# Kernel optimization log

Measured on AMD Instinct MI355X. Metric: run time of the kernel, lower is better.

Reference implementation:

```python
import jax, jax.numpy as jnp
import numpy as np
from jax import lax

B = 256
C1 = 256          # conv1 channels
NUM_CAPS = 32     # primary capsule types
CAP_DIM = 8       # primary capsule dim
NUM_PRIMARY = NUM_CAPS * 6 * 6  # 1152
NUM_OUT = 10
OUT_DIM = 16
NUM_ROUTING = 3


def squash(v):
    # v: (..., d)
    sq = jnp.sum(v * v, axis=-1, keepdims=True)
    scale = sq / (1.0 + sq)
    return scale * v / jnp.sqrt(sq + 1e-8)


def setup_inputs() -> dict:
    key = jax.random.key(0)
    k = jax.random.split(key, 6)
    x = jax.random.normal(k[0], (B, 1, 28, 28), dtype=jnp.float32)
    # kaiming fan_out init for convs
    conv1_w = jax.random.normal(k[1], (C1, 1, 9, 9), dtype=jnp.float32) * np.sqrt(2.0 / (C1 * 81))
    conv1_b = jnp.zeros((C1,), dtype=jnp.float32)
    pc_out = NUM_CAPS * CAP_DIM  # 256
    pc_w = jax.random.normal(k[2], (pc_out, C1, 9, 9), dtype=jnp.float32) * np.sqrt(2.0 / (pc_out * 81))
    pc_b = jnp.zeros((pc_out,), dtype=jnp.float32)
    W_digit = jax.random.normal(k[3], (NUM_PRIMARY, CAP_DIM, NUM_OUT, OUT_DIM), dtype=jnp.float32) * 0.01
    return {"x": x, "conv1_w": conv1_w, "conv1_b": conv1_b,
            "pc_w": pc_w, "pc_b": pc_b, "W_digit": W_digit}


def _conv(x, w, b, stride):
    y = lax.conv_general_dilated(x, w, (stride, stride), 'VALID',
                                 dimension_numbers=('NCHW', 'OIHW', 'NCHW'))
    return y + b[None, :, None, None]


def reference(x, conv1_w, conv1_b, pc_w, pc_b, W_digit):
    # conv1 + ReLU: (B,1,28,28) -> (B,256,20,20)
    h = jax.nn.relu(_conv(x, conv1_w, conv1_b, 1))
    # primary caps conv: -> (B, 256, 6, 6)
    p = _conv(h, pc_w, pc_b, 2)
    bsz, _, oh, ow = p.shape
    # (B, num_caps, cap_dim, H, W) -> (B, num_caps, H, W, cap_dim) -> (B, N, d)
    p = p.reshape(bsz, NUM_CAPS, CAP_DIM, oh, ow)
    p = jnp.transpose(p, (0, 1, 3, 4, 2)).reshape(bsz, NUM_CAPS * oh * ow, CAP_DIM)
    u = squash(p)  # (B, 1152, 8)
    # dynamic routing
    u_hat = jnp.einsum('bid,idjo->bijo', u, W_digit)  # (B, 1152, 10, 16)
    b_logits = jnp.zeros((bsz, NUM_PRIMARY, NUM_OUT, 1), dtype=u_hat.dtype)
    v = None
    for it in range(NUM_ROUTING):
        c = jax.nn.softmax(b_logits, axis=2)
        s = jnp.sum(c * u_hat, axis=1)          # (B, 10, 16)
        v = squash(s)
        if it < NUM_ROUTING - 1:
            agreement = jnp.sum(u_hat * v[:, None, :, :], axis=-1, keepdims=True)
            b_logits = b_logits + agreement
    return v
```

## Files before the change

### kernel.cpp

```cpp
#include <hip/hip_runtime.h>
#include <hip/hip_bf16.h>

#define NI 1152

typedef __attribute__((ext_vector_type(8))) _Float16 f16x8;
typedef __attribute__((ext_vector_type(4))) float f32x4;
typedef __attribute__((ext_vector_type(8))) unsigned short u16x8;
typedef __attribute__((ext_vector_type(4))) unsigned short u16x4;

static const size_t UHAT_OFF = 0;
static const size_t W6_OFF   = 0;
static const size_t H3_OFF   = 10747904UL;
static const size_t WT1_OFF  = 63176704UL;
static const size_t PP_OFF   = 63259648UL;
static const size_t U_OFF    = 94371840UL;
static const size_t SP_OFF   = 103809024UL;
static const size_t L_OFF    = 127401984UL;
static const size_t V_OFF    = 139198464UL;

__device__ __forceinline__ unsigned short f2bf(float x) {
    unsigned u = __builtin_bit_cast(unsigned, x);
    u += 0x7fffu + ((u >> 16) & 1u);
    return (unsigned short)(u >> 16);
}
__device__ __forceinline__ float bf2f(unsigned short h) {
    return __builtin_bit_cast(float, (unsigned)h << 16);
}
__device__ __forceinline__ void atomAddF(float* p, float v) {
    __hip_atomic_fetch_add(p, v, __ATOMIC_RELAXED, __HIP_MEMORY_SCOPE_AGENT);
}

__global__ __launch_bounds__(256) void k_prep_w(const float* __restrict__ pcw,
                                                _Float16* __restrict__ w6) {
    __shared__ float sl[5184];
    int oc  = blockIdx.x;
    int ic0 = blockIdx.y * 64;
    const float* src = pcw + (size_t)oc * 20736 + (size_t)ic0 * 81;
    for (int j = threadIdx.x; j < 5184; j += 256) sl[j] = src[j];
    __syncthreads();
    int og = oc >> 4, fr = oc & 15;
    for (int t = threadIdx.x; t < 5184; t += 256) {
        int tap = t >> 6, i = t & 63;
        int ic = ic0 + i;
        int ks = ic >> 5, kch = (ic >> 3) & 3, icl = ic & 7;
        int lane = kch * 16 + fr;
        w6[(((size_t)(tap * 8 + ks) * 16 + og) * 64 + lane) * 8 + icl] =
            (_Float16)sl[i * 81 + tap];
    }
}

__global__ void k_transpose_w1(const float* __restrict__ w, float* __restrict__ wT) {
    int t = blockIdx.x, oc = threadIdx.x;
    wT[t * 256 + oc] = w[oc * 81 + t];
}

__global__ __launch_bounds__(256) void k_conv1(const float* __restrict__ x,
                                               const float* __restrict__ wT1,
                                               const float* __restrict__ bias,
                                               _Float16* __restrict__ h3) {
    __shared__ _Float16 hs[2][20][256];
    int b  = blockIdx.y;
    int rp = blockIdx.x;
    int oc = threadIdx.x;
    int oy0 = rp * 2;
    const float* xb = x + (size_t)b * 784;
    float bv = bias[oc];
    float acc0[20], acc1[20];
#pragma unroll
    for (int i = 0; i < 20; ++i) { acc0[i] = bv; acc1[i] = bv; }
    for (int ky = 0; ky < 9; ++ky) {
        const float* r0 = xb + (oy0 + ky) * 28;
        const float* r1 = r0 + 28;
        float x0[28], x1[28];
#pragma unroll
        for (int c = 0; c < 28; ++c) { x0[c] = r0[c]; x1[c] = r1[c]; }
#pragma unroll
        for (int kx = 0; kx < 9; ++kx) {
            float w = wT1[(ky * 9 + kx) * 256 + oc];
#pragma unroll
            for (int px = 0; px < 20; ++px) {
                acc0[px] += x0[px + kx] * w;
                acc1[px] += x1[px + kx] * w;
            }
        }
    }
#pragma unroll
    for (int px = 0; px < 20; ++px) {
        hs[0][px][oc] = (_Float16)fmaxf(acc0[px], 0.f);
        hs[1][px][oc] = (_Float16)fmaxf(acc1[px], 0.f);
    }
    __syncthreads();
    for (int cid = threadIdx.x; cid < 1280; cid += 256) {
        int kp = cid & 31;
        int pos = cid >> 5;
        int ry = pos / 20, px2 = pos % 20;
        int ks = kp >> 2, p = kp & 3;
        f16x8 val = *(const f16x8*)&hs[ry][px2][ks * 32 + p * 8];
        _Float16* dst = h3 + ((size_t)((ks * 400 + (oy0 + ry) * 20 + px2) * 4 + p) * 256 + b) * 8;
        *(f16x8*)dst = val;
    }
}

__global__ __launch_bounds__(256, 2) void k_conv2_direct(
    const _Float16* __restrict__ h3, const _Float16* __restrict__ w6,
    float* __restrict__ pp) {
    const int blk = blockIdx.x;
    const int ks = blk & 7;
    const int rest = blk >> 3;
    const int mt = rest % 72;
    const int nt = rest / 72;
    const int pos = mt >> 1, bhalf = mt & 1;
    const int py = pos / 6, px = pos % 6;
    const int l = threadIdx.x & 63;
    const int w = threadIdx.x >> 6;
    const int wm = w >> 1, wn = w & 1;
    const int p = l >> 4, fr = l & 15;

    const _Float16* abase = h3 + (size_t)ks * 3276800 + p * 2048 +
                            (bhalf * 128 + wm * 64 + fr) * 8;
    const _Float16* bbase = w6 + (nt * 8 + wn * 4) * 512 + l * 8;

    f16x8 a[3][4], b[3][4];
    f32x4 acc[4][4];
    const f32x4 z = {0.f, 0.f, 0.f, 0.f};
#pragma unroll
    for (int mi = 0; mi < 4; ++mi)
#pragma unroll
        for (int ni = 0; ni < 4; ++ni) acc[mi][ni] = z;

#define LOADAB(buf, tap)                                                       \
    do {                                                                       \
        const int _t = (tap);                                                  \
        const int _y = _t / 9, _x = _t - _y * 9;                               \
        const _Float16* _ab = abase + ((2 * py + _y) * 20 + (2 * px + _x)) * 8192; \
        a[buf][0] = *(const f16x8*)(_ab);                                      \
        a[buf][1] = *(const f16x8*)(_ab + 128);                                \
        a[buf][2] = *(const f16x8*)(_ab + 256);                                \
        a[buf][3] = *(const f16x8*)(_ab + 384);                                \
        const _Float16* _bb = bbase + (size_t)(_t * 8 + ks) * 8192;            \
        b[buf][0] = *(const f16x8*)(_bb);                                      \
        b[buf][1] = *(const f16x8*)(_bb + 512);                                \
        b[buf][2] = *(const f16x8*)(_bb + 1024);                               \
        b[buf][3] = *(const f16x8*)(_bb + 1536);                               \
    } while (0)

#define MFMA_ALL(buf)                                                          \
    do {                                                                       \
        _Pragma("unroll") for (int mi = 0; mi < 4; ++mi)                       \
            _Pragma("unroll") for (int ni = 0; ni < 4; ++ni)                   \
                acc[mi][ni] = __builtin_amdgcn_mfma_f32_16x16x32_f16(          \
                    a[buf][mi], b[buf][ni], acc[buf == buf ? mi : mi][ni], 0, 0, 0); \
    } while (0)

#undef MFMA_ALL
#define MFMA_ALL(buf)                                                          \
    do {                                                                       \
        _Pragma("unroll") for (int mi = 0; mi < 4; ++mi)                       \
            _Pragma("unroll") for (int ni = 0; ni < 4; ++ni)                   \
                acc[mi][ni] = __builtin_amdgcn_mfma_f32_16x16x32_f16(          \
                    a[buf][mi], b[buf][ni], acc[mi][ni], 0, 0, 0);             \
    } while (0)

    LOADAB(0, 0);
    LOADAB(1, 1);
    for (int k = 0; k < 27; ++k) {
        const int t0 = 3 * k;
        LOADAB(2, t0 + 2);
        MFMA_ALL(0);
        if (t0 + 3 < 81) LOADAB(0, t0 + 3);
        MFMA_ALL(1);
        if (t0 + 4 < 81) LOADAB(1, t0 + 4);
        MFMA_ALL(2);
    }
#undef LOADAB
#undef MFMA_ALL

    const int row0 = (l >> 4) * 4;
    const int ncol = l & 15;
#pragma unroll
    for (int mi = 0; mi < 4; ++mi)
#pragma unroll
        for (int ni = 0; ni < 4; ++ni) {
            int n = nt * 128 + wn * 64 + ni * 16 + ncol;
#pragma unroll
            for (int reg = 0; reg < 4; ++reg) {
                int m = pos * 256 + bhalf * 128 + wm * 64 + mi * 16 + row0 + reg;
                atomAddF(&pp[(size_t)m * 256 + n], acc[mi][ni][reg]);
            }
        }
}

__global__ __launch_bounds__(256) void k_sum_squash2(const float* __restrict__ pp,
                                                     const float* __restrict__ bias,
                                                     float* __restrict__ u) {
    int m = blockIdx.x * 8 + (threadIdx.x >> 5);
    int cap = threadIdx.x & 31;
    const float* p0 = pp + (size_t)m * 256 + cap * 8;
    float s[8], sq = 0.f;
#pragma unroll
    for (int d = 0; d < 8; ++d) {
        float a = p0[d] + bias[cap * 8 + d];
        sq += a * a; s[d] = a;
    }
    float scale = sq / ((1.0f + sq) * sqrtf(sq + 1e-8f));
    int pos = m >> 8, b = m & 255;
    int i = cap * 36 + pos;
    float* up = u + ((size_t)i * 256 + b) * 8;
    ((float4*)up)[0] = make_float4(scale * s[0], scale * s[1], scale * s[2], scale * s[3]);
    ((float4*)up)[1] = make_float4(scale * s[4], scale * s[5], scale * s[6], scale * s[7]);
}

__global__ __launch_bounds__(256) void k_build_uhat(const float* __restrict__ u,
                                                    const float* __restrict__ W,
                                                    unsigned short* __restrict__ UH) {
    __shared__ float Ws[1280];
    int i = blockIdx.x;
    for (int t = threadIdx.x; t < 1280; t += 256) Ws[t] = W[(size_t)i * 1280 + t];
    __syncthreads();
    int b = threadIdx.x;
    const float* uptr = u + ((size_t)i * 256 + b) * 8;
    float u8[8];
    ((float4*)u8)[0] = ((const float4*)uptr)[0];
    ((float4*)u8)[1] = ((const float4*)uptr)[1];
#pragma unroll
    for (int j = 0; j < 10; ++j) {
        float o16[16];
#pragma unroll
        for (int o = 0; o < 16; ++o) o16[o] = 0.f;
#pragma unroll
        for (int d = 0; d < 8; ++d) {
            const float* wp = Ws + d * 160 + j * 16;
#pragma unroll
            for (int o = 0; o < 16; ++o) o16[o] += u8[d] * wp[o];
        }
        u16x8 h0, h1;
#pragma unroll
        for (int o = 0; o < 8; ++o) { h0[o] = f2bf(o16[o]); h1[o] = f2bf(o16[8 + o]); }
        unsigned short* dst = UH + ((size_t)(i * 10 + j) * 256 + b) * 16;
        *(u16x8*)dst = h0;
        *(u16x8*)(dst + 8) = h1;
    }
}

__global__ __launch_bounds__(256) void k_route_s0(const unsigned short* __restrict__ UH,
                                                  float* __restrict__ SP) {
    int it = blockIdx.x, bt = blockIdx.y;
    int b0 = bt * 64, i0 = it * 8;
    int b_l = threadIdx.x & 63;
    int og = __builtin_amdgcn_readfirstlane((int)(threadIdx.x >> 6));
    float acc[10][4];
#pragma unroll
    for (int j = 0; j < 10; ++j)
#pragma unroll
        for (int o = 0; o < 4; ++o) acc[j][o] = 0.f;
    for (int li = 0; li < 8; ++li) {
        const unsigned short* up = UH + ((size_t)(i0 + li) * 10 * 256 + b0 + b_l) * 16 + og * 4;
#pragma unroll
        for (int j = 0; j < 10; ++j) {
            u16x4 t = *(const u16x4*)(up + j * 4096);
#pragma unroll
            for (int o = 0; o < 4; ++o) acc[j][o] += bf2f(t[o]);
        }
    }
    float* sp = SP + ((size_t)it * 256 + b0 + b_l) * 160 + og * 4;
#pragma unroll
    for (int j = 0; j < 10; ++j)
        *(float4*)(sp + j * 16) = make_float4(0.1f * acc[j][0], 0.1f * acc[j][1],
                                              0.1f * acc[j][2], 0.1f * acc[j][3]);
}

__global__ __launch_bounds__(256) void k_route_as(float* __restrict__ L,
                                                  const unsigned short* __restrict__ UH,
                                                  const float* __restrict__ V,
                                                  float* __restrict__ SP,
                                                  int add, int storeL) {
    __shared__ float VL[64][165];
    __shared__ float LG[64][81];
    int it = blockIdx.x, bt = blockIdx.y;
    int b0 = bt * 64, i0 = it * 8;
    int b_l = threadIdx.x & 63;
    int ig = __builtin_amdgcn_readfirstlane((int)(threadIdx.x >> 6));
    int b_r = threadIdx.x >> 2, part = threadIdx.x & 3;
    {
        const float4* vsrc = (const float4*)(V + (size_t)(b0 + b_r) * 160 + part * 40);
#pragma unroll
        for (int q = 0; q < 10; ++q) {
            float4 vv = vsrc[q]; int c = part * 40 + q * 4;
            VL[b_r][c] = vv.x; VL[b_r][c + 1] = vv.y; VL[b_r][c + 2] = vv.z; VL[b_r][c + 3] = vv.w;
        }
        if (add) {
            const float4* lsrc = (const float4*)(L + (size_t)(b0 + b_r) * 11520 + i0 * 10 + part * 20);
#pragma unroll
            for (int q = 0; q < 5; ++q) {
                float4 t = lsrc[q]; int c = part * 20 + q * 4;
                LG[b_r][c] = t.x; LG[b_r][c + 1] = t.y; LG[b_r][c + 2] = t.z; LG[b_r][c + 3] = t.w;
            }
        }
    }
    __syncthreads();
#pragma unroll
    for (int ii = 0; ii < 2; ++ii) {
        int il = ig * 2 + ii;
        int i = i0 + il;
        const unsigned short* up = UH + ((size_t)i * 10 * 256 + b0 + b_l) * 16;
#pragma unroll
        for (int j = 0; j < 10; ++j) {
            u16x8 ua = *(const u16x8*)(up + j * 4096);
            u16x8 ub = *(const u16x8*)(up + j * 4096 + 8);
            float a = 0.f;
#pragma unroll
            for (int o = 0; o < 8; ++o) a += bf2f(ua[o]) * VL[b_l][j * 16 + o];
#pragma unroll
            for (int o = 0; o < 8; ++o) a += bf2f(ub[o]) * VL[b_l][j * 16 + 8 + o];
            float base = add ? LG[b_l][il * 10 + j] : 0.f;
            LG[b_l][il * 10 + j] = base + a;
        }
    }
    __syncthreads();
    if (storeL) {
        float4* ldst = (float4*)(L + (size_t)(b0 + b_r) * 11520 + i0 * 10 + part * 20);
#pragma unroll
        for (int q = 0; q < 5; ++q) {
            int c = part * 20 + q * 4;
            ldst[q] = make_float4(LG[b_r][c], LG[b_r][c + 1], LG[b_r][c + 2], LG[b_r][c + 3]);
        }
    }
    float acc[10][4];
#pragma unroll
    for (int j = 0; j < 10; ++j)
#pragma unroll
        for (int o = 0; o < 4; ++o) acc[j][o] = 0.f;
    for (int li = 0; li < 8; ++li) {
        float lg[10];
#pragma unroll
        for (int j = 0; j < 10; ++j) lg[j] = LG[b_l][li * 10 + j];
        float m = lg[0];
#pragma unroll
        for (int j = 1; j < 10; ++j) m = fmaxf(m, lg[j]);
        float e[10], ssum = 0.f;
#pragma unroll
        for (int j = 0; j < 10; ++j) { e[j] = __expf(lg[j] - m); ssum += e[j]; }
        float inv = 1.0f / ssum;
        const unsigned short* up = UH + ((size_t)(i0 + li) * 10 * 256 + b0 + b_l) * 16 + ig * 4;
#pragma unroll
        for (int j = 0; j < 10; ++j) {
            float cj = e[j] * inv;
            u16x4 t = *(const u16x4*)(up + j * 4096);
#pragma unroll
            for (int o = 0; o < 4; ++o) acc[j][o] += cj * bf2f(t[o]);
        }
    }
    float* sp = SP + ((size_t)it * 256 + b0 + b_l) * 160 + ig * 4;
#pragma unroll
    for (int j = 0; j < 10; ++j)
        *(float4*)(sp + j * 16) = make_float4(acc[j][0], acc[j][1], acc[j][2], acc[j][3]);
}

__global__ __launch_bounds__(256) void k_route_v(const float* __restrict__ SP,
                                                 float* __restrict__ vout) {
    int n = blockIdx.x * 256 + threadIdx.x;
    float ssum = 0.f;
    for (int t = 0; t < 144; ++t) ssum += SP[(size_t)t * 40960 + n];
    float sq = ssum * ssum;
    float tot = sq;
#pragma unroll
    for (int mask = 1; mask < 16; mask <<= 1) tot += __shfl_xor(tot, mask, 64);
    float scale = tot / ((1.0f + tot) * sqrtf(tot + 1e-8f));
    vout[n] = scale * ssum;
}

extern "C" void kernel_launch(void* const* d_in, const int* in_sizes, int n_in,
                              void* d_out, int out_size, void* d_ws, size_t ws_size,
                              hipStream_t stream) {
    (void)in_sizes; (void)n_in; (void)out_size; (void)ws_size;
    const float* x   = (const float*)d_in[0];
    const float* c1w = (const float*)d_in[1];
    const float* c1b = (const float*)d_in[2];
    const float* pcw = (const float*)d_in[3];
    const float* pcb = (const float*)d_in[4];
    const float* Wd  = (const float*)d_in[5];
    float* out = (float*)d_out;
    char* wsb  = (char*)d_ws;

    unsigned short* uh = (unsigned short*)(wsb + UHAT_OFF);
    _Float16* w6 = (_Float16*)(wsb + W6_OFF);
    _Float16* h3 = (_Float16*)(wsb + H3_OFF);
    float* wT1 = (float*)(wsb + WT1_OFF);
    float* pp  = (float*)(wsb + PP_OFF);
    float* u   = (float*)(wsb + U_OFF);
    float* sp  = (float*)(wsb + SP_OFF);
    float* lg  = (float*)(wsb + L_OFF);
    float* v   = (float*)(wsb + V_OFF);

    hipMemsetAsync(pp, 0, (size_t)9216 * 256 * sizeof(float), stream);

    k_prep_w<<<dim3(256, 4), 256, 0, stream>>>(pcw, w6);
    k_transpose_w1<<<81, 256, 0, stream>>>(c1w, wT1);
    k_conv1<<<dim3(10, 256), 256, 0, stream>>>(x, wT1, c1b, h3);
    k_conv2_direct<<<dim3(1152), 256, 0, stream>>>(h3, w6, pp);
    k_sum_squash2<<<1152, 256, 0, stream>>>(pp, pcb, u);
    k_build_uhat<<<1152, 256, 0, stream>>>(u, Wd, uh);

    k_route_s0<<<dim3(144, 4), 256, 0, stream>>>(uh, sp);
    k_route_v<<<160, 256, 0, stream>>>(sp, v);
    k_route_as<<<dim3(144, 4), 256, 0, stream>>>(lg, uh, v, sp, 0, 1);
    k_route_v<<<160, 256, 0, stream>>>(sp, v);
    k_route_as<<<dim3(144, 4), 256, 0, stream>>>(lg, uh, v, sp, 1, 0);
    k_route_v<<<160, 256, 0, stream>>>(sp, out);
}
```

Measured before the change: 438.2 us.

## Stage conv2 operand tiles through LDS with async global_load_lds double buffering

Replaces the per-wave direct global-to-register loads in the conv2 implicit GEMM with block-cooperative global_load_lds copies into double-buffered shared memory, so each A and B tile is fetched once per block and shared between waves. A barrier per tap synchronises the buffers. The occupancy hint is raised from 2 to 3 blocks per CU to offset the smaller register footprint. This adds LDS traffic and a per-tap sync, and its correctness depends on the exact lane-to-LDS layout of global_load_lds.

```diff
diff --git a/kernel.cpp b/kernel.cpp
--- a/kernel.cpp
+++ b/kernel.cpp
@@ -101,9 +101,12 @@
     }
 }
 
-__global__ __launch_bounds__(256, 2) void k_conv2_direct(
+__global__ __launch_bounds__(256, 3) void k_conv2_direct(
     const _Float16* __restrict__ h3, const _Float16* __restrict__ w6,
     float* __restrict__ pp) {
+    __shared__ _Float16 Asl[2 * 4096];
+    __shared__ _Float16 Bsl[2 * 4096];
+
     const int blk = blockIdx.x;
     const int ks = blk & 7;
     const int rest = blk >> 3;
@@ -111,16 +114,37 @@
     const int nt = rest / 72;
     const int pos = mt >> 1, bhalf = mt & 1;
     const int py = pos / 6, px = pos % 6;
-    const int l = threadIdx.x & 63;
-    const int w = threadIdx.x >> 6;
+    const int tid = threadIdx.x;
+    const int l = tid & 63;
+    const int w = tid >> 6;
+    const int wu = __builtin_amdgcn_readfirstlane(w);
     const int wm = w >> 1, wn = w & 1;
     const int p = l >> 4, fr = l & 15;
 
-    const _Float16* abase = h3 + (size_t)ks * 3276800 + p * 2048 +
-                            (bhalf * 128 + wm * 64 + fr) * 8;
-    const _Float16* bbase = w6 + (nt * 8 + wn * 4) * 512 + l * 8;
-
-    f16x8 a[3][4], b[3][4];
+    const _Float16* aglb = h3 + (size_t)ks * 3276800 + (tid >> 7) * 2048 +
+                           (bhalf * 128 + (tid & 127)) * 8;
+    const _Float16* bglb = w6 + (size_t)ks * 8192 + nt * 4096 + tid * 8;
+
+#define STAGE(buf, aoff, boff)                                                     \
+    do {                                                                           \
+        const _Float16* _ga = aglb + (aoff);                                       \
+        const _Float16* _gb = bglb + (boff);                                       \
+        _Float16* _la = Asl + (buf) * 4096 + wu * 512;                             \
+        _Float16* _lb = Bsl + (buf) * 4096 + wu * 512;                             \
+        __builtin_amdgcn_global_load_lds(                                          \
+            (const __attribute__((address_space(1))) void*)_ga,                    \
+            (__attribute__((address_space(3))) void*)_la, 16, 0, 0);               \
+        __builtin_amdgcn_global_load_lds(                                          \
+            (const __attribute__((address_space(1))) void*)(_ga + 4096),           \
+            (__attribute__((address_space(3))) void*)(_la + 2048), 16, 0, 0);      \
+        __builtin_amdgcn_global_load_lds(                                          \
+            (const __attribute__((address_space(1))) void*)_gb,                    \
+            (__attribute__((address_space(3))) void*)(_lb), 16, 0, 0);             \
+        __builtin_amdgcn_global_load_lds(                                          \
+            (const __attribute__((address_space(1))) void*)(_gb + 2048),           \
+            (__attribute__((address_space(3))) void*)(_lb + 2048), 16, 0, 0);      \
+    } while (0)
+
     f32x4 acc[4][4];
     const f32x4 z = {0.f, 0.f, 0.f, 0.f};
 #pragma unroll
@@ -128,52 +152,38 @@
 #pragma unroll
         for (int ni = 0; ni < 4; ++ni) acc[mi][ni] = z;
 
-#define LOADAB(buf, tap)                                                       \
-    do {                                                                       \
-        const int _t = (tap);                                                  \
-        const int _y = _t / 9, _x = _t - _y * 9;                               \
-        const _Float16* _ab = abase + ((2 * py + _y) * 20 + (2 * px + _x)) * 8192; \
-        a[buf][0] = *(const f16x8*)(_ab);                                      \
-        a[buf][1] = *(const f16x8*)(_ab + 128);                                \
-        a[buf][2] = *(const f16x8*)(_ab + 256);                                \
-        a[buf][3] = *(const f16x8*)(_ab + 384);                                \
-        const _Float16* _bb = bbase + (size_t)(_t * 8 + ks) * 8192;            \
-        b[buf][0] = *(const f16x8*)(_bb);                                      \
-        b[buf][1] = *(const f16x8*)(_bb + 512);                                \
-        b[buf][2] = *(const f16x8*)(_bb + 1024);                               \
-        b[buf][3] = *(const f16x8*)(_bb + 1536);                               \
+#define COMPUTE(buf)                                                               \
+    do {                                                                           \
+        f16x8 af[4], bf[4];                                                        \
+        const _Float16* _ab = Asl + (buf) * 4096 + p * 1024 + (wm * 64 + fr) * 8;  \
+        const _Float16* _bb = Bsl + (buf) * 4096 + wn * 2048 + l * 8;              \
+        _Pragma("unroll") for (int mi = 0; mi < 4; ++mi)                           \
+            af[mi] = *(const f16x8*)(_ab + mi * 128);                              \
+        _Pragma("unroll") for (int ni = 0; ni < 4; ++ni)                           \
+            bf[ni] = *(const f16x8*)(_bb + ni * 512);                              \
+        _Pragma("unroll") for (int mi = 0; mi < 4; ++mi)                           \
+            _Pragma("unroll") for (int ni = 0; ni < 4; ++ni)                       \
+                acc[mi][ni] = __builtin_amdgcn_mfma_f32_16x16x32_f16(              \
+                    af[mi], bf[ni], acc[mi][ni], 0, 0, 0);                         \
     } while (0)
 
-#define MFMA_ALL(buf)                                                          \
-    do {                                                                       \
-        _Pragma("unroll") for (int mi = 0; mi < 4; ++mi)                       \
-            _Pragma("unroll") for (int ni = 0; ni < 4; ++ni)                   \
-                acc[mi][ni] = __builtin_amdgcn_mfma_f32_16x16x32_f16(          \
-                    a[buf][mi], b[buf][ni], acc[buf == buf ? mi : mi][ni], 0, 0, 0); \
-    } while (0)
-
-#undef MFMA_ALL
-#define MFMA_ALL(buf)                                                          \
-    do {                                                                       \
-        _Pragma("unroll") for (int mi = 0; mi < 4; ++mi)                       \
-            _Pragma("unroll") for (int ni = 0; ni < 4; ++ni)                   \
-                acc[mi][ni] = __builtin_amdgcn_mfma_f32_16x16x32_f16(          \
-                    a[buf][mi], b[buf][ni], acc[mi][ni], 0, 0, 0);             \
-    } while (0)
-
-    LOADAB(0, 0);
-    LOADAB(1, 1);
-    for (int k = 0; k < 27; ++k) {
-        const int t0 = 3 * k;
-        LOADAB(2, t0 + 2);
-        MFMA_ALL(0);
-        if (t0 + 3 < 81) LOADAB(0, t0 + 3);
-        MFMA_ALL(1);
-        if (t0 + 4 < 81) LOADAB(1, t0 + 4);
-        MFMA_ALL(2);
-    }
-#undef LOADAB
-#undef MFMA_ALL
+    int win = (2 * py) * 20 + 2 * px;
+    STAGE(0, (size_t)win * 8192, 0);
+    __syncthreads();
+    int wx = 0;
+    size_t boff = 0;
+    int buf = 0;
+    for (int t = 0; t < 80; ++t) {
+        if (wx == 8) { wx = 0; win += 12; } else { ++wx; win += 1; }
+        boff += 65536;
+        STAGE(buf ^ 1, (size_t)win * 8192, boff);
+        COMPUTE(buf);
+        __syncthreads();
+        buf ^= 1;
+    }
+    COMPUTE(buf);
+#undef STAGE
+#undef COMPUTE
 
     const int row0 = (l >> 4) * 4;
     const int ncol = l & 15;
```

Result: slower. 483.2 us (+10.3%).
